# Optimization experiments

Hardware: AMD Instinct MI355X
Metric: run time of the kernel (lower is better)

Reference implementation:

```python
import jax, jax.numpy as jnp
import numpy as np

N_NODES = 50000
N_EDGES = 800000
IN_DIM = 64
HID = 128
OUT_DIM = 64
T_HIST = 8


def setup_inputs() -> dict:
    key = jax.random.key(0)
    ks = jax.random.split(key, 12)
    s = 0.05
    return {
        "node_feats": jax.random.normal(ks[0], (N_NODES, IN_DIM), jnp.float32),
        "history_feats": jax.random.normal(ks[1], (N_NODES, T_HIST, HID), jnp.float32),
        "src": jax.random.randint(ks[2], (N_EDGES,), 0, N_NODES, jnp.int32),
        "dst": jax.random.randint(ks[3], (N_EDGES,), 0, N_NODES, jnp.int32),
        # SAGEConv params (fc_self, fc_neigh share bias as in DGL)
        "W_self": jax.random.normal(ks[4], (IN_DIM, HID), jnp.float32) * s,
        "W_neigh": jax.random.normal(ks[5], (IN_DIM, HID), jnp.float32) * s,
        "b_sage": jnp.zeros((HID,), jnp.float32),
        # LSTM params, PyTorch gate order [i, f, g, o]
        "w_ih": jax.random.normal(ks[6], (HID, 4 * HID), jnp.float32) * s,
        "w_hh": jax.random.normal(ks[7], (HID, 4 * HID), jnp.float32) * s,
        "b_lstm": jnp.zeros((4 * HID,), jnp.float32),
        # classifier
        "W_cls": jax.random.normal(ks[8], (HID, OUT_DIM), jnp.float32) * s,
        "b_cls": jnp.zeros((OUT_DIM,), jnp.float32),
    }


def _lstm_last(x, w_ih, w_hh, b):
    # x: [N, T, H] -> last hidden state [N, H]
    N, T, H = x.shape

    def step(carry, xt):
        h, c = carry
        gates = xt @ w_ih + h @ w_hh + b  # [N, 4H]
        i, f, g, o = jnp.split(gates, 4, axis=-1)
        c = jax.nn.sigmoid(f) * c + jax.nn.sigmoid(i) * jnp.tanh(g)
        h = jax.nn.sigmoid(o) * jnp.tanh(c)
        return (h, c), None

    h0 = jnp.zeros((N, H), x.dtype)
    (h, _), _ = jax.lax.scan(step, (h0, h0), jnp.swapaxes(x, 0, 1))
    return h


def reference(node_feats, history_feats, src, dst, W_self, W_neigh, b_sage,
              w_ih, w_hh, b_lstm, W_cls, b_cls):
    N = node_feats.shape[0]
    # SAGEConv mean aggregation: mean of in-neighbor features per dst node
    msg_sum = jax.ops.segment_sum(node_feats[src], dst, num_segments=N)
    deg = jax.ops.segment_sum(jnp.ones((src.shape[0],), node_feats.dtype),
                              dst, num_segments=N)
    h_neigh = msg_sum / jnp.maximum(deg, 1.0)[:, None]
    h_struct = node_feats @ W_self + h_neigh @ W_neigh + b_sage  # [N, HID]
    # LSTM over history, take last timestep
    h_temp = _lstm_last(history_feats, w_ih, w_hh, b_lstm)  # [N, HID]
    h_combined = h_struct + h_temp
    return h_combined @ W_cls + b_cls  # [N, OUT_DIM]
```

## Files before the change

kernel.cpp:

```cpp
#include <hip/hip_runtime.h>
#include <hip/hip_bf16.h>
#include <stdint.h>

#define N_NODES 50000
#define N_EDGES 800000
#define IN_DIM 64
#define HID 128
#define OUT_DIM 64
#define T_HIST 8

#define NB_SCAN ((N_NODES + 1023) / 1024)

typedef __attribute__((ext_vector_type(8))) short short8;
typedef __attribute__((ext_vector_type(4))) float f32x4;

__device__ __forceinline__ unsigned short f2bf(float x) {
  unsigned int u = __builtin_bit_cast(unsigned int, x);
  unsigned int r = (u + 0x7FFFu + ((u >> 16) & 1u)) >> 16;
  return (unsigned short)r;
}
__device__ __forceinline__ short8 cvt8(float4 a, float4 b) {
  unsigned int w0, w1, w2, w3;
  asm("v_cvt_pk_bf16_f32 %0, %1, %2" : "=v"(w0) : "v"(a.x), "v"(a.y));
  asm("v_cvt_pk_bf16_f32 %0, %1, %2" : "=v"(w1) : "v"(a.z), "v"(a.w));
  asm("v_cvt_pk_bf16_f32 %0, %1, %2" : "=v"(w2) : "v"(b.x), "v"(b.y));
  asm("v_cvt_pk_bf16_f32 %0, %1, %2" : "=v"(w3) : "v"(b.z), "v"(b.w));
  struct { unsigned int a, b, c, d; } s{w0, w1, w2, w3};
  return __builtin_bit_cast(short8, s);
}
__device__ __forceinline__ float sigm(float x) {
  float e = __builtin_amdgcn_exp2f(-1.4426950408889634f * x);
  return __builtin_amdgcn_rcpf(1.f + e);
}
__device__ __forceinline__ float tanh_f(float x) {
  float e = __builtin_amdgcn_exp2f(2.8853900817779268f * x);
  return 1.f - 2.f * __builtin_amdgcn_rcpf(e + 1.f);
}

__global__ void pc_kernel(const float* __restrict__ w_ih, const float* __restrict__ w_hh,
                          const float* __restrict__ W_cls,
                          const float* __restrict__ W_self, const float* __restrict__ W_neigh,
                          const float* __restrict__ b_sage, const float* __restrict__ b_cls,
                          const int* __restrict__ dst,
                          unsigned short* __restrict__ Wt2, unsigned short* __restrict__ Wc2,
                          float* __restrict__ Wsc, float* __restrict__ Wnc,
                          float* __restrict__ bc1, int* __restrict__ cnt) {
  int tid = blockIdx.x * blockDim.x + threadIdx.x;
  int stride = gridDim.x * blockDim.x;
  for (int e = tid; e < N_EDGES; e += stride) atomicAdd(&cnt[dst[e]], 1);
  for (int idx = tid; idx < 256 * 512; idx += stride) {
    int i = idx & 7;
    int lane = (idx >> 3) & 63;
    int F = idx >> 9;
    int q = F >> 5, g = (F >> 3) & 3, kk = F & 7;
    int c = g * 128 + q * 16 + (lane & 15);
    int k = kk * 32 + (lane >> 4) * 8 + i;
    float v = (k < 128) ? w_ih[k * 512 + c] : w_hh[(k - 128) * 512 + c];
    Wt2[idx] = f2bf(v);
  }
  for (int idx = tid; idx < 16 * 512; idx += stride) {
    int i = idx & 7;
    int lane = (idx >> 3) & 63;
    int F = idx >> 9;
    int cb = F >> 2, kk = F & 3;
    int col = cb * 16 + (lane & 15);
    int k = kk * 32 + (lane >> 4) * 8 + i;
    Wc2[idx] = f2bf(W_cls[k * 64 + col]);
  }
  for (int idx = tid; idx < 64 * 64; idx += stride) {
    int k = idx >> 6, c = idx & 63;
    float as = 0.f, an = 0.f;
    for (int m = 0; m < 128; m++) {
      float wc = W_cls[m * 64 + c];
      as += W_self[k * 128 + m] * wc;
      an += W_neigh[k * 128 + m] * wc;
    }
    Wsc[idx] = as;
    Wnc[idx] = an;
  }
  for (int c = tid; c < 64; c += stride) {
    float acc = b_cls[c];
    for (int m = 0; m < 128; m++) acc += b_sage[m] * W_cls[m * 64 + c];
    bc1[c] = acc;
  }
}

__global__ __launch_bounds__(256) void scan1_kernel(const int* __restrict__ cnt,
                                                    int* __restrict__ lexcl, int* __restrict__ btot) {
  __shared__ int sh[256];
  int tid = threadIdx.x;
  int base = blockIdx.x * 1024 + tid * 4;
  int v[4];
  #pragma unroll
  for (int q = 0; q < 4; q++) {
    int i = base + q;
    v[q] = (i < N_NODES) ? cnt[i] : 0;
  }
  int tsum = v[0] + v[1] + v[2] + v[3];
  sh[tid] = tsum;
  __syncthreads();
  int val = tsum;
  for (int off = 1; off < 256; off <<= 1) {
    int x = (tid >= off) ? sh[tid - off] : 0;
    __syncthreads();
    val += x;
    sh[tid] = val;
    __syncthreads();
  }
  int ex = val - tsum;
  if (tid == 255) btot[blockIdx.x] = val;
  #pragma unroll
  for (int q = 0; q < 4; q++) {
    int i = base + q;
    if (i < N_NODES) lexcl[i] = ex;
    ex += v[q];
  }
}

__global__ __launch_bounds__(1024) void scan3_kernel(const int* __restrict__ lexcl,
                                                     const int* __restrict__ btot,
                                                     int* __restrict__ rowstart, int* __restrict__ cursor) {
  int b = blockIdx.x;
  int bs = 0;
  for (int j = 0; j < b; j++) bs += btot[j];
  int i = b * 1024 + threadIdx.x;
  if (i < N_NODES) {
    int rs = lexcl[i] + bs;
    rowstart[i] = rs;
    cursor[i] = rs;
  }
}

__global__ void fill_kernel(const int* __restrict__ src, const int* __restrict__ dst,
                            int* __restrict__ cursor, int* __restrict__ esrc) {
  int e = blockIdx.x * blockDim.x + threadIdx.x;
  if (e < N_EDGES) {
    int d = dst[e];
    int pos = atomicAdd(&cursor[d], 1);
    esrc[pos] = src[e];
  }
}

#define HS_TILE 32
__global__ __launch_bounds__(512) void hstruct_kernel(
    const float* __restrict__ nf, const int* __restrict__ esrc,
    const int* __restrict__ rowstart, const int* __restrict__ cnt,
    const float* __restrict__ Wsc, const float* __restrict__ Wnc, const float* __restrict__ bc1,
    float* __restrict__ out1) {
  __shared__ float s_nf[HS_TILE][IN_DIM + 1];
  __shared__ float s_hn[HS_TILE][IN_DIM + 1];
  int tid = threadIdx.x;
  int node0 = blockIdx.x * HS_TILE;
  for (int i = tid; i < HS_TILE * IN_DIM; i += 512) {
    int r = i >> 6, k = i & 63;
    int node = node0 + r;
    s_nf[r][k] = (node < N_NODES) ? nf[node * 64 + k] : 0.f;
  }
  int wv = tid >> 6, lane = tid & 63;
  for (int r = wv; r < HS_TILE; r += 8) {
    int node = node0 + r;
    float a0 = 0.f, a1 = 0.f, a2 = 0.f, a3 = 0.f;
    int n = 0;
    if (node < N_NODES) {
      n = cnt[node];
      int st = rowstart[node];
      int j = 0;
      for (; j + 4 <= n; j += 4) {
        int s0 = esrc[st + j], s1 = esrc[st + j + 1];
        int s2 = esrc[st + j + 2], s3 = esrc[st + j + 3];
        a0 += nf[s0 * 64 + lane];
        a1 += nf[s1 * 64 + lane];
        a2 += nf[s2 * 64 + lane];
        a3 += nf[s3 * 64 + lane];
      }
      for (; j < n; j++) a0 += nf[esrc[st + j] * 64 + lane];
    }
    s_hn[r][lane] = (a0 + a1 + a2 + a3) * __builtin_amdgcn_rcpf(fmaxf((float)n, 1.f));
  }
  __syncthreads();
  int r = tid & 31;
  int c0 = (tid >> 5) * 4;
  float accs[4] = {0.f, 0.f, 0.f, 0.f};
  for (int k = 0; k < IN_DIM; k++) {
    float a = s_nf[r][k];
    float b = s_hn[r][k];
    float4 w1 = *(const float4*)&Wsc[k * 64 + c0];
    float4 w2 = *(const float4*)&Wnc[k * 64 + c0];
    accs[0] += a * w1.x + b * w2.x;
    accs[1] += a * w1.y + b * w2.y;
    accs[2] += a * w1.z + b * w2.z;
    accs[3] += a * w1.w + b * w2.w;
  }
  int node = node0 + r;
  if (node < N_NODES) {
    #pragma unroll
    for (int i = 0; i < 4; i++)
      out1[(size_t)node * 64 + c0 + i] = accs[i] + bc1[c0 + i];
  }
}

#define LB 64
__global__ __launch_bounds__(512, 2) void lstm_kernel(
    const float* __restrict__ hist,
    const unsigned short* __restrict__ Wt2,
    const unsigned short* __restrict__ Wc2,
    const float* __restrict__ b_lstm,
    const float* __restrict__ out1,
    float* __restrict__ out)
{
  __shared__ alignas(16) unsigned short Abuf[2][64 * 256];

  const int tid = threadIdx.x;
  const int lane = tid & 63;
  const int w = tid >> 6;
  const int l15 = lane & 15;
  const int l4 = lane >> 4;
  const int base = blockIdx.x * LB;
  const int jj = w * 16 + l15;

  short8 Bfr[4][8];
  #pragma unroll
  for (int g = 0; g < 4; g++)
    #pragma unroll
    for (int kk = 0; kk < 8; kk++)
      Bfr[g][kk] = *(const short8*)&Wt2[((w * 32 + g * 8 + kk) * 64 + lane) * 8];

  const float bi  = b_lstm[jj];
  const float bf_ = b_lstm[128 + jj];
  const float bg  = b_lstm[256 + jj];
  const float bo  = b_lstm[384 + jj];

  float c_st[16];
  #pragma unroll
  for (int i = 0; i < 16; i++) c_st[i] = 0.f;

  for (int u = tid; u < 64 * 16; u += 512) {
    int row = u >> 4;
    int kbh = u & 15;
    short8 z = {0,0,0,0,0,0,0,0};
    *(short8*)&Abuf[0][row * 256 + 128 + kbh * 8] = z;
  }
  #pragma unroll
  for (int i2 = 0; i2 < 2; i2++) {
    int u = tid + (i2 << 9);
    int row = u >> 4;
    int kb = u & 15;
    int node = base + row;
    float4 x0 = make_float4(0.f,0.f,0.f,0.f), x1 = make_float4(0.f,0.f,0.f,0.f);
    if (node < N_NODES) {
      const float4* p = (const float4*)&hist[(size_t)node * (T_HIST * HID) + kb * 8];
      x0 = p[0]; x1 = p[1];
    }
    int sb = (kb & 8) | ((kb & 7) ^ (row & 7));
    *(short8*)&Abuf[0][row * 256 + sb * 8] = cvt8(x0, x1);
  }
  __syncthreads();

  float4 xp[4];

  #pragma unroll
  for (int t = 0; t < T_HIST - 1; t++) {
    unsigned short* Acur = &Abuf[t & 1][0];
    unsigned short* Anxt = &Abuf[(t & 1) ^ 1][0];

    #pragma unroll
    for (int i2 = 0; i2 < 2; i2++) {
      int u = tid + (i2 << 9);
      int row = u >> 4;
      int kb = u & 15;
      int node = base + row;
      if (node < N_NODES) {
        const float4* p = (const float4*)&hist[(size_t)node * (T_HIST * HID) + (t + 1) * HID + kb * 8];
        xp[i2 * 2]     = p[0];
        xp[i2 * 2 + 1] = p[1];
      } else {
        xp[i2 * 2]     = make_float4(0.f,0.f,0.f,0.f);
        xp[i2 * 2 + 1] = make_float4(0.f,0.f,0.f,0.f);
      }
    }

    #pragma unroll
    for (int rb = 0; rb < 4; rb++) {
      f32x4 acc[4];
      #pragma unroll
      for (int g = 0; g < 4; g++) { f32x4 z = {0.f,0.f,0.f,0.f}; acc[g] = z; }
      #pragma unroll
      for (int kk = 0; kk < 8; kk++) {
        int row = rb * 16 + l15;
        int kb = kk * 4 + l4;
        int sb = (kb & 24) | ((kb & 7) ^ (row & 7));
        short8 a = *(const short8*)&Acur[row * 256 + sb * 8];
        #pragma unroll
        for (int g = 0; g < 4; g++)
          acc[g] = __builtin_amdgcn_mfma_f32_16x16x32_bf16(a, Bfr[g][kk], acc[g], 0, 0, 0);
      }
      #pragma unroll
      for (int reg = 0; reg < 4; reg++) {
        int r = rb * 4 + reg;
        float gi = sigm(acc[0][reg] + bi);
        float gf = sigm(acc[1][reg] + bf_);
        float gg = tanh_f(acc[2][reg] + bg);
        float go = sigm(acc[3][reg] + bo);
        float c = gf * c_st[r] + gi * gg;
        c_st[r] = c;
        float h = go * tanh_f(c);
        int row = rb * 16 + l4 * 4 + reg;
        int kb = 16 + (jj >> 3);
        int sb = (kb & 24) | ((kb & 7) ^ (row & 7));
        Anxt[row * 256 + sb * 8 + (jj & 7)] = f2bf(h);
      }
      __builtin_amdgcn_sched_barrier(0);
    }

    #pragma unroll
    for (int i2 = 0; i2 < 2; i2++) {
      int u = tid + (i2 << 9);
      int row = u >> 4;
      int kb = u & 15;
      int sb = (kb & 8) | ((kb & 7) ^ (row & 7));
      *(short8*)&Anxt[row * 256 + sb * 8] = cvt8(xp[i2 * 2], xp[i2 * 2 + 1]);
    }
    __syncthreads();
  }

  {
    unsigned short* Acur = &Abuf[1][0];
    unsigned short* Anxt = &Abuf[0][0];

    #pragma unroll
    for (int rb = 0; rb < 4; rb++) {
      f32x4 acc[4];
      #pragma unroll
      for (int g = 0; g < 4; g++) { f32x4 z = {0.f,0.f,0.f,0.f}; acc[g] = z; }
      #pragma unroll
      for (int kk = 0; kk < 8; kk++) {
        int row = rb * 16 + l15;
        int kb = kk * 4 + l4;
        int sb = (kb & 24) | ((kb & 7) ^ (row & 7));
        short8 a = *(const short8*)&Acur[row * 256 + sb * 8];
        #pragma unroll
        for (int g = 0; g < 4; g++)
          acc[g] = __builtin_amdgcn_mfma_f32_16x16x32_bf16(a, Bfr[g][kk], acc[g], 0, 0, 0);
      }
      #pragma unroll
      for (int reg = 0; reg < 4; reg++) {
        int r = rb * 4 + reg;
        float gi = sigm(acc[0][reg] + bi);
        float gf = sigm(acc[1][reg] + bf_);
        float gg = tanh_f(acc[2][reg] + bg);
        float go = sigm(acc[3][reg] + bo);
        float c = gf * c_st[r] + gi * gg;
        float h = go * tanh_f(c);
        int row = rb * 16 + l4 * 4 + reg;
        int kb = jj >> 3;
        int sb = (kb & 8) | ((kb & 7) ^ (row & 7));
        Anxt[row * 256 + sb * 8 + (jj & 7)] = f2bf(h);
      }
      __builtin_amdgcn_sched_barrier(0);
    }
    __syncthreads();

    #pragma unroll
    for (int fi = 0; fi < 2; fi++) {
      int f = w * 2 + fi;
      int rbo = f >> 2, cbo = f & 3;
      int col = cbo * 16 + l15;
      float ov[4];
      #pragma unroll
      for (int reg = 0; reg < 4; reg++) {
        int row = rbo * 16 + l4 * 4 + reg;
        int node = base + row;
        ov[reg] = (node < N_NODES) ? out1[(size_t)node * OUT_DIM + col] : 0.f;
      }
      f32x4 o = {0.f, 0.f, 0.f, 0.f};
      #pragma unroll
      for (int kk = 0; kk < 4; kk++) {
        short8 bv = *(const short8*)&Wc2[((cbo * 4 + kk) * 64 + lane) * 8];
        int row = rbo * 16 + l15;
        int kb = kk * 4 + l4;
        int sb = (kb & 8) | ((kb & 7) ^ (row & 7));
        short8 a = *(const short8*)&Anxt[row * 256 + sb * 8];
        o = __builtin_amdgcn_mfma_f32_16x16x32_bf16(a, bv, o, 0, 0, 0);
      }
      #pragma unroll
      for (int reg = 0; reg < 4; reg++) {
        int row = rbo * 16 + l4 * 4 + reg;
        int node = base + row;
        if (node < N_NODES) out[(size_t)node * OUT_DIM + col] = o[reg] + ov[reg];
      }
    }
  }
}

extern "C" void kernel_launch(void* const* d_in, const int* in_sizes, int n_in,
                              void* d_out, int out_size, void* d_ws, size_t ws_size,
                              hipStream_t stream) {
  (void)in_sizes; (void)n_in; (void)out_size; (void)ws_size;
  const float* node_feats = (const float*)d_in[0];
  const float* hist       = (const float*)d_in[1];
  const int*   src        = (const int*)d_in[2];
  const int*   dst        = (const int*)d_in[3];
  const float* W_self     = (const float*)d_in[4];
  const float* W_neigh    = (const float*)d_in[5];
  const float* b_sage     = (const float*)d_in[6];
  const float* w_ih       = (const float*)d_in[7];
  const float* w_hh       = (const float*)d_in[8];
  const float* b_lstm     = (const float*)d_in[9];
  const float* W_cls      = (const float*)d_in[10];
  const float* b_cls      = (const float*)d_in[11];
  float* out = (float*)d_out;

  char* ws = (char*)d_ws;
  int* cnt        = (int*)(ws);
  int* lexcl      = (int*)(ws + 200192);
  int* rowstart   = (int*)(ws + 400384);
  int* cursor     = (int*)(ws + 600576);
  int* btot       = (int*)(ws + 800768);
  int* esrc       = (int*)(ws + 801792);
  float* out1     = (float*)(ws + 4001792);
  unsigned short* Wt2 = (unsigned short*)(ws + 16801792);
  unsigned short* Wc2 = (unsigned short*)(ws + 17063936);
  float* Wsc      = (float*)(ws + 17080320);
  float* Wnc      = (float*)(ws + 17096704);
  float* bc1      = (float*)(ws + 17113088);

  hipMemsetAsync(cnt, 0, 200000, stream);
  pc_kernel<<<1024, 256, 0, stream>>>(w_ih, w_hh, W_cls, W_self, W_neigh, b_sage, b_cls,
                                      dst, Wt2, Wc2, Wsc, Wnc, bc1, cnt);
  scan1_kernel<<<NB_SCAN, 256, 0, stream>>>(cnt, lexcl, btot);
  scan3_kernel<<<NB_SCAN, 1024, 0, stream>>>(lexcl, btot, rowstart, cursor);
  fill_kernel<<<(N_EDGES + 255) / 256, 256, 0, stream>>>(src, dst, cursor, esrc);
  hstruct_kernel<<<(N_NODES + HS_TILE - 1) / HS_TILE, 512, 0, stream>>>(
      node_feats, esrc, rowstart, cnt, Wsc, Wnc, bc1, out1);
  lstm_kernel<<<(N_NODES + LB - 1) / LB, 512, 0, stream>>>(
      hist, Wt2, Wc2, b_lstm, out1, out);
}
```

Measured before the change: 363.9 us.

## Fuse SAGE neighbor aggregation and projection into LSTM classifier kernel

Removes the separate hstruct kernel and its out1 intermediate. The LSTM kernel now gathers neighbor means and self features per node and writes them as bf16 into unused columns of the shared A tile. An extra set of MFMAs then applies the pre-combined (W_self|W_neigh)@W_cls matrix, which is stored in bf16 fragment layout. This saves one launch and the write and re-read of a 50000x64 float buffer, but the irregular gather is now serialized inside the LSTM blocks and node and neighbor features are rounded to bf16.

New measurement: 376.5 us. 1.03x slower.

```diff
diff --git a/kernel.cpp b/kernel.cpp
--- a/kernel.cpp
+++ b/kernel.cpp
@@ -43,7 +43,7 @@
                           const float* __restrict__ b_sage, const float* __restrict__ b_cls,
                           const int* __restrict__ dst,
                           unsigned short* __restrict__ Wt2, unsigned short* __restrict__ Wc2,
-                          float* __restrict__ Wsc, float* __restrict__ Wnc,
+                          unsigned short* __restrict__ Wsnc2,
                           float* __restrict__ bc1, int* __restrict__ cnt) {
   int tid = blockIdx.x * blockDim.x + threadIdx.x;
   int stride = gridDim.x * blockDim.x;
@@ -67,16 +67,17 @@
     int k = kk * 32 + (lane >> 4) * 8 + i;
     Wc2[idx] = f2bf(W_cls[k * 64 + col]);
   }
-  for (int idx = tid; idx < 64 * 64; idx += stride) {
-    int k = idx >> 6, c = idx & 63;
-    float as = 0.f, an = 0.f;
-    for (int m = 0; m < 128; m++) {
-      float wc = W_cls[m * 64 + c];
-      as += W_self[k * 128 + m] * wc;
-      an += W_neigh[k * 128 + m] * wc;
-    }
-    Wsc[idx] = as;
-    Wnc[idx] = an;
+  for (int idx = tid; idx < 16 * 512; idx += stride) {
+    int i = idx & 7;
+    int lane = (idx >> 3) & 63;
+    int F = idx >> 9;
+    int cb = F >> 2, kk = F & 3;
+    int col = cb * 16 + (lane & 15);
+    int k = kk * 32 + (lane >> 4) * 8 + i;
+    const float* Wrow = (k < 64) ? &W_self[k * 128] : &W_neigh[(k - 64) * 128];
+    float v = 0.f;
+    for (int m = 0; m < 128; m++) v += Wrow[m] * W_cls[m * 64 + col];
+    Wsnc2[idx] = f2bf(v);
   }
   for (int c = tid; c < 64; c += stride) {
     float acc = b_cls[c];
@@ -141,71 +142,18 @@
   }
 }
 
-#define HS_TILE 32
-__global__ __launch_bounds__(512) void hstruct_kernel(
-    const float* __restrict__ nf, const int* __restrict__ esrc,
-    const int* __restrict__ rowstart, const int* __restrict__ cnt,
-    const float* __restrict__ Wsc, const float* __restrict__ Wnc, const float* __restrict__ bc1,
-    float* __restrict__ out1) {
-  __shared__ float s_nf[HS_TILE][IN_DIM + 1];
-  __shared__ float s_hn[HS_TILE][IN_DIM + 1];
-  int tid = threadIdx.x;
-  int node0 = blockIdx.x * HS_TILE;
-  for (int i = tid; i < HS_TILE * IN_DIM; i += 512) {
-    int r = i >> 6, k = i & 63;
-    int node = node0 + r;
-    s_nf[r][k] = (node < N_NODES) ? nf[node * 64 + k] : 0.f;
-  }
-  int wv = tid >> 6, lane = tid & 63;
-  for (int r = wv; r < HS_TILE; r += 8) {
-    int node = node0 + r;
-    float a0 = 0.f, a1 = 0.f, a2 = 0.f, a3 = 0.f;
-    int n = 0;
-    if (node < N_NODES) {
-      n = cnt[node];
-      int st = rowstart[node];
-      int j = 0;
-      for (; j + 4 <= n; j += 4) {
-        int s0 = esrc[st + j], s1 = esrc[st + j + 1];
-        int s2 = esrc[st + j + 2], s3 = esrc[st + j + 3];
-        a0 += nf[s0 * 64 + lane];
-        a1 += nf[s1 * 64 + lane];
-        a2 += nf[s2 * 64 + lane];
-        a3 += nf[s3 * 64 + lane];
-      }
-      for (; j < n; j++) a0 += nf[esrc[st + j] * 64 + lane];
-    }
-    s_hn[r][lane] = (a0 + a1 + a2 + a3) * __builtin_amdgcn_rcpf(fmaxf((float)n, 1.f));
-  }
-  __syncthreads();
-  int r = tid & 31;
-  int c0 = (tid >> 5) * 4;
-  float accs[4] = {0.f, 0.f, 0.f, 0.f};
-  for (int k = 0; k < IN_DIM; k++) {
-    float a = s_nf[r][k];
-    float b = s_hn[r][k];
-    float4 w1 = *(const float4*)&Wsc[k * 64 + c0];
-    float4 w2 = *(const float4*)&Wnc[k * 64 + c0];
-    accs[0] += a * w1.x + b * w2.x;
-    accs[1] += a * w1.y + b * w2.y;
-    accs[2] += a * w1.z + b * w2.z;
-    accs[3] += a * w1.w + b * w2.w;
-  }
-  int node = node0 + r;
-  if (node < N_NODES) {
-    #pragma unroll
-    for (int i = 0; i < 4; i++)
-      out1[(size_t)node * 64 + c0 + i] = accs[i] + bc1[c0 + i];
-  }
-}
-
 #define LB 64
 __global__ __launch_bounds__(512, 2) void lstm_kernel(
     const float* __restrict__ hist,
     const unsigned short* __restrict__ Wt2,
     const unsigned short* __restrict__ Wc2,
+    const unsigned short* __restrict__ Wsnc2,
     const float* __restrict__ b_lstm,
-    const float* __restrict__ out1,
+    const float* __restrict__ nf,
+    const int* __restrict__ esrc,
+    const int* __restrict__ rowstart,
+    const int* __restrict__ cnt,
+    const float* __restrict__ bc1,
     float* __restrict__ out)
 {
   __shared__ alignas(16) unsigned short Abuf[2][64 * 256];
@@ -358,6 +306,43 @@
       }
       __builtin_amdgcn_sched_barrier(0);
     }
+
+    float nfreg[8], hnreg[8];
+    #pragma unroll
+    for (int rr = 0; rr < 8; rr++) {
+      int node = base + w * 8 + rr;
+      nfreg[rr] = (node < N_NODES) ? nf[node * 64 + lane] : 0.f;
+    }
+    for (int rr = 0; rr < 8; rr++) {
+      int node = base + w * 8 + rr;
+      float a0 = 0.f, a1 = 0.f, a2 = 0.f, a3 = 0.f;
+      int n = 0;
+      if (node < N_NODES) {
+        n = cnt[node];
+        int st = rowstart[node];
+        int j = 0;
+        for (; j + 4 <= n; j += 4) {
+          int s0 = esrc[st + j], s1 = esrc[st + j + 1];
+          int s2 = esrc[st + j + 2], s3 = esrc[st + j + 3];
+          a0 += nf[s0 * 64 + lane];
+          a1 += nf[s1 * 64 + lane];
+          a2 += nf[s2 * 64 + lane];
+          a3 += nf[s3 * 64 + lane];
+        }
+        for (; j < n; j++) a0 += nf[esrc[st + j] * 64 + lane];
+      }
+      hnreg[rr] = (a0 + a1 + a2 + a3) * __builtin_amdgcn_rcpf(fmaxf((float)n, 1.f));
+    }
+    #pragma unroll
+    for (int rr = 0; rr < 8; rr++) {
+      int row = w * 8 + rr;
+      int kbn = 16 + (lane >> 3);
+      int sbn = (kbn & 24) | ((kbn & 7) ^ (row & 7));
+      Anxt[row * 256 + sbn * 8 + (lane & 7)] = f2bf(nfreg[rr]);
+      int kbh = 24 + (lane >> 3);
+      int sbh = (kbh & 24) | ((kbh & 7) ^ (row & 7));
+      Anxt[row * 256 + sbh * 8 + (lane & 7)] = f2bf(hnreg[rr]);
+    }
     __syncthreads();
 
     #pragma unroll
@@ -365,13 +350,6 @@
       int f = w * 2 + fi;
       int rbo = f >> 2, cbo = f & 3;
       int col = cbo * 16 + l15;
-      float ov[4];
-      #pragma unroll
-      for (int reg = 0; reg < 4; reg++) {
-        int row = rbo * 16 + l4 * 4 + reg;
-        int node = base + row;
-        ov[reg] = (node < N_NODES) ? out1[(size_t)node * OUT_DIM + col] : 0.f;
-      }
       f32x4 o = {0.f, 0.f, 0.f, 0.f};
       #pragma unroll
       for (int kk = 0; kk < 4; kk++) {
@@ -383,10 +361,20 @@
         o = __builtin_amdgcn_mfma_f32_16x16x32_bf16(a, bv, o, 0, 0, 0);
       }
       #pragma unroll
+      for (int kk = 0; kk < 4; kk++) {
+        short8 bv = *(const short8*)&Wsnc2[((cbo * 4 + kk) * 64 + lane) * 8];
+        int row = rbo * 16 + l15;
+        int kb = 16 + kk * 4 + l4;
+        int sb = (kb & 24) | ((kb & 7) ^ (row & 7));
+        short8 a = *(const short8*)&Anxt[row * 256 + sb * 8];
+        o = __builtin_amdgcn_mfma_f32_16x16x32_bf16(a, bv, o, 0, 0, 0);
+      }
+      float bcl = bc1[col];
+      #pragma unroll
       for (int reg = 0; reg < 4; reg++) {
         int row = rbo * 16 + l4 * 4 + reg;
         int node = base + row;
-        if (node < N_NODES) out[(size_t)node * OUT_DIM + col] = o[reg] + ov[reg];
+        if (node < N_NODES) out[(size_t)node * OUT_DIM + col] = o[reg] + bcl;
       }
     }
   }
@@ -417,21 +405,17 @@
   int* cursor     = (int*)(ws + 600576);
   int* btot       = (int*)(ws + 800768);
   int* esrc       = (int*)(ws + 801792);
-  float* out1     = (float*)(ws + 4001792);
-  unsigned short* Wt2 = (unsigned short*)(ws + 16801792);
-  unsigned short* Wc2 = (unsigned short*)(ws + 17063936);
-  float* Wsc      = (float*)(ws + 17080320);
-  float* Wnc      = (float*)(ws + 17096704);
-  float* bc1      = (float*)(ws + 17113088);
+  unsigned short* Wt2   = (unsigned short*)(ws + 4001792);
+  unsigned short* Wc2   = (unsigned short*)(ws + 4263936);
+  unsigned short* Wsnc2 = (unsigned short*)(ws + 4280320);
+  float* bc1      = (float*)(ws + 4296704);
 
   hipMemsetAsync(cnt, 0, 200000, stream);
   pc_kernel<<<1024, 256, 0, stream>>>(w_ih, w_hh, W_cls, W_self, W_neigh, b_sage, b_cls,
-                                      dst, Wt2, Wc2, Wsc, Wnc, bc1, cnt);
+                                      dst, Wt2, Wc2, Wsnc2, bc1, cnt);
   scan1_kernel<<<NB_SCAN, 256, 0, stream>>>(cnt, lexcl, btot);
   scan3_kernel<<<NB_SCAN, 1024, 0, stream>>>(lexcl, btot, rowstart, cursor);
   fill_kernel<<<(N_EDGES + 255) / 256, 256, 0, stream>>>(src, dst, cursor, esrc);
-  hstruct_kernel<<<(N_NODES + HS_TILE - 1) / HS_TILE, 512, 0, stream>>>(
-      node_feats, esrc, rowstart, cnt, Wsc, Wnc, bc1, out1);
   lstm_kernel<<<(N_NODES + LB - 1) / LB, 512, 0, stream>>>(
-      hist, Wt2, Wc2, b_lstm, out1, out);
-}
+      hist, Wt2, Wc2, Wsnc2, b_lstm, node_feats, esrc, rowstart, cnt, bc1, out);
+}
```

## Split LSTM gates across wave pairs with LDS gate exchange, 1024-thread blocks

Applied to the files above, without the earlier changes.

The LSTM kernel now runs 16 waves per block, each wave pair sharing a 16-column slice, with each wave computing two of the four gate groups. The half of the gate results a wave does not own is exchanged through a new shared-memory buffer, so each wave applies the nonlinearities for half of the rows. This halves the per-wave B-fragment registers and cell state, aiming for higher occupancy and more parallelism. The cost is an extra barrier per timestep, extra LDS traffic and usage, and the time loop is no longer unrolled.

New measurement: 444.5 us. +22.1%, slower.

```diff
diff --git a/kernel.cpp b/kernel.cpp
--- a/kernel.cpp
+++ b/kernel.cpp
@@ -200,7 +200,7 @@
 }
 
 #define LB 64
-__global__ __launch_bounds__(512, 2) void lstm_kernel(
+__global__ __launch_bounds__(1024, 4) void lstm_kernel(
     const float* __restrict__ hist,
     const unsigned short* __restrict__ Wt2,
     const unsigned short* __restrict__ Wc2,
@@ -209,42 +209,36 @@
     float* __restrict__ out)
 {
   __shared__ alignas(16) unsigned short Abuf[2][64 * 256];
+  __shared__ float Gbuf[2][2][32][132];
 
   const int tid = threadIdx.x;
   const int lane = tid & 63;
   const int w = tid >> 6;
+  const int q = w >> 1;
+  const int h = w & 1;
   const int l15 = lane & 15;
   const int l4 = lane >> 4;
   const int base = blockIdx.x * LB;
-  const int jj = w * 16 + l15;
-
-  short8 Bfr[4][8];
+  const int jj = q * 16 + l15;
+
+  short8 Bfr[2][8];
   #pragma unroll
-  for (int g = 0; g < 4; g++)
+  for (int gg = 0; gg < 2; gg++)
     #pragma unroll
     for (int kk = 0; kk < 8; kk++)
-      Bfr[g][kk] = *(const short8*)&Wt2[((w * 32 + g * 8 + kk) * 64 + lane) * 8];
-
-  const float bi  = b_lstm[jj];
-  const float bf_ = b_lstm[128 + jj];
-  const float bg  = b_lstm[256 + jj];
-  const float bo  = b_lstm[384 + jj];
-
-  float c_st[16];
+      Bfr[gg][kk] = *(const short8*)&Wt2[((q * 32 + (2 * h + gg) * 8 + kk) * 64 + lane) * 8];
+
+  const float bA = b_lstm[(2 * h + 0) * 128 + jj];
+  const float bB = b_lstm[(2 * h + 1) * 128 + jj];
+
+  float c_st[8];
   #pragma unroll
-  for (int i = 0; i < 16; i++) c_st[i] = 0.f;
-
-  for (int u = tid; u < 64 * 16; u += 512) {
-    int row = u >> 4;
-    int kbh = u & 15;
+  for (int i = 0; i < 8; i++) c_st[i] = 0.f;
+
+  {
+    int row = tid >> 4, kb = tid & 15;
     short8 z = {0,0,0,0,0,0,0,0};
-    *(short8*)&Abuf[0][row * 256 + 128 + kbh * 8] = z;
-  }
-  #pragma unroll
-  for (int i2 = 0; i2 < 2; i2++) {
-    int u = tid + (i2 << 9);
-    int row = u >> 4;
-    int kb = u & 15;
+    *(short8*)&Abuf[0][row * 256 + 128 + kb * 8] = z;
     int node = base + row;
     float4 x0 = make_float4(0.f,0.f,0.f,0.f), x1 = make_float4(0.f,0.f,0.f,0.f);
     if (node < N_NODES) {
@@ -256,138 +250,110 @@
   }
   __syncthreads();
 
-  float4 xp[4];
-
-  #pragma unroll
-  for (int t = 0; t < T_HIST - 1; t++) {
+  #pragma unroll 1
+  for (int t = 0; t < T_HIST; t++) {
     unsigned short* Acur = &Abuf[t & 1][0];
     unsigned short* Anxt = &Abuf[(t & 1) ^ 1][0];
 
-    #pragma unroll
-    for (int i2 = 0; i2 < 2; i2++) {
-      int u = tid + (i2 << 9);
-      int row = u >> 4;
-      int kb = u & 15;
-      int node = base + row;
-      if (node < N_NODES) {
-        const float4* p = (const float4*)&hist[(size_t)node * (T_HIST * HID) + (t + 1) * HID + kb * 8];
-        xp[i2 * 2]     = p[0];
-        xp[i2 * 2 + 1] = p[1];
-      } else {
-        xp[i2 * 2]     = make_float4(0.f,0.f,0.f,0.f);
-        xp[i2 * 2 + 1] = make_float4(0.f,0.f,0.f,0.f);
-      }
-    }
+    f32x4 ownA[2][2];
 
     #pragma unroll
     for (int rb = 0; rb < 4; rb++) {
-      f32x4 acc[4];
-      #pragma unroll
-      for (int g = 0; g < 4; g++) { f32x4 z = {0.f,0.f,0.f,0.f}; acc[g] = z; }
+      f32x4 a0 = {0.f,0.f,0.f,0.f}, a1 = {0.f,0.f,0.f,0.f};
       #pragma unroll
       for (int kk = 0; kk < 8; kk++) {
         int row = rb * 16 + l15;
         int kb = kk * 4 + l4;
         int sb = (kb & 24) | ((kb & 7) ^ (row & 7));
         short8 a = *(const short8*)&Acur[row * 256 + sb * 8];
+        a0 = __builtin_amdgcn_mfma_f32_16x16x32_bf16(a, Bfr[0][kk], a0, 0, 0, 0);
+        a1 = __builtin_amdgcn_mfma_f32_16x16x32_bf16(a, Bfr[1][kk], a1, 0, 0, 0);
+      }
+      bool own = (h == 0) ? (rb < 2) : (rb >= 2);
+      if (own) {
+        ownA[rb & 1][0] = a0;
+        ownA[rb & 1][1] = a1;
+      } else {
+        int r32b = (h == 0) ? (rb - 2) * 16 : rb * 16;
         #pragma unroll
-        for (int g = 0; g < 4; g++)
-          acc[g] = __builtin_amdgcn_mfma_f32_16x16x32_bf16(a, Bfr[g][kk], acc[g], 0, 0, 0);
+        for (int reg = 0; reg < 4; reg++) {
+          int r32 = r32b + l4 * 4 + reg;
+          Gbuf[h][0][r32][jj] = a0[reg] + bA;
+          Gbuf[h][1][r32][jj] = a1[reg] + bB;
+        }
       }
+      __builtin_amdgcn_sched_barrier(0);
+    }
+    __syncthreads();
+
+    #pragma unroll
+    for (int p = 0; p < 2; p++) {
       #pragma unroll
       for (int reg = 0; reg < 4; reg++) {
-        int r = rb * 4 + reg;
-        float gi = sigm(acc[0][reg] + bi);
-        float gf = sigm(acc[1][reg] + bf_);
-        float gg = tanh_f(acc[2][reg] + bg);
-        float go = sigm(acc[3][reg] + bo);
-        float c = gf * c_st[r] + gi * gg;
-        c_st[r] = c;
-        float h = go * tanh_f(c);
-        int row = rb * 16 + l4 * 4 + reg;
-        int kb = 16 + (jj >> 3);
-        int sb = (kb & 24) | ((kb & 7) ^ (row & 7));
-        Anxt[row * 256 + sb * 8 + (jj & 7)] = f2bf(h);
+        int r32 = p * 16 + l4 * 4 + reg;
+        int row = h * 32 + r32;
+        int ci = p * 4 + reg;
+        float o0 = ownA[p][0][reg] + bA;
+        float o1 = ownA[p][1][reg] + bB;
+        float g0 = Gbuf[1 - h][0][r32][jj];
+        float g1 = Gbuf[1 - h][1][r32][jj];
+        float gi, gf, gg_, go;
+        if (h == 0) { gi = sigm(o0); gf = sigm(o1); gg_ = tanh_f(g0); go = sigm(g1); }
+        else        { gi = sigm(g0); gf = sigm(g1); gg_ = tanh_f(o0); go = sigm(o1); }
+        float c = gf * c_st[ci] + gi * gg_;
+        c_st[ci] = c;
+        float hv = go * tanh_f(c);
+        if (t < T_HIST - 1) {
+          int kb = 16 + (jj >> 3);
+          int sb = (kb & 24) | ((kb & 7) ^ (row & 7));
+          Anxt[row * 256 + sb * 8 + (jj & 7)] = f2bf(hv);
+        } else {
+          int kb = jj >> 3;
+          int sb = (kb & 8) | ((kb & 7) ^ (row & 7));
+          Anxt[row * 256 + sb * 8 + (jj & 7)] = f2bf(hv);
+        }
       }
-      __builtin_amdgcn_sched_barrier(0);
-    }
-
-    #pragma unroll
-    for (int i2 = 0; i2 < 2; i2++) {
-      int u = tid + (i2 << 9);
-      int row = u >> 4;
-      int kb = u & 15;
+    }
+    if (t < T_HIST - 1) {
+      int row = tid >> 4, kb = tid & 15;
+      int node = base + row;
+      float4 x0 = make_float4(0.f,0.f,0.f,0.f), x1 = make_float4(0.f,0.f,0.f,0.f);
+      if (node < N_NODES) {
+        const float4* p = (const float4*)&hist[(size_t)node * (T_HIST * HID) + (t + 1) * HID + kb * 8];
+        x0 = p[0]; x1 = p[1];
+      }
       int sb = (kb & 8) | ((kb & 7) ^ (row & 7));
-      *(short8*)&Anxt[row * 256 + sb * 8] = cvt8(xp[i2 * 2], xp[i2 * 2 + 1]);
+      *(short8*)&Anxt[row * 256 + sb * 8] = cvt8(x0, x1);
     }
     __syncthreads();
   }
 
   {
-    unsigned short* Acur = &Abuf[1][0];
-    unsigned short* Anxt = &Abuf[0][0];
-
-    #pragma unroll
-    for (int rb = 0; rb < 4; rb++) {
-      f32x4 acc[4];
-      #pragma unroll
-      for (int g = 0; g < 4; g++) { f32x4 z = {0.f,0.f,0.f,0.f}; acc[g] = z; }
-      #pragma unroll
-      for (int kk = 0; kk < 8; kk++) {
-        int row = rb * 16 + l15;
-        int kb = kk * 4 + l4;
-        int sb = (kb & 24) | ((kb & 7) ^ (row & 7));
-        short8 a = *(const short8*)&Acur[row * 256 + sb * 8];
-        #pragma unroll
-        for (int g = 0; g < 4; g++)
-          acc[g] = __builtin_amdgcn_mfma_f32_16x16x32_bf16(a, Bfr[g][kk], acc[g], 0, 0, 0);
-      }
-      #pragma unroll
-      for (int reg = 0; reg < 4; reg++) {
-        int r = rb * 4 + reg;
-        float gi = sigm(acc[0][reg] + bi);
-        float gf = sigm(acc[1][reg] + bf_);
-        float gg = tanh_f(acc[2][reg] + bg);
-        float go = sigm(acc[3][reg] + bo);
-        float c = gf * c_st[r] + gi * gg;
-        float h = go * tanh_f(c);
-        int row = rb * 16 + l4 * 4 + reg;
-        int kb = jj >> 3;
-        int sb = (kb & 8) | ((kb & 7) ^ (row & 7));
-        Anxt[row * 256 + sb * 8 + (jj & 7)] = f2bf(h);
-      }
-      __builtin_amdgcn_sched_barrier(0);
-    }
-    __syncthreads();
-
-    #pragma unroll
-    for (int fi = 0; fi < 2; fi++) {
-      int f = w * 2 + fi;
-      int rbo = f >> 2, cbo = f & 3;
-      int col = cbo * 16 + l15;
-      float ov[4];
-      #pragma unroll
-      for (int reg = 0; reg < 4; reg++) {
-        int row = rbo * 16 + l4 * 4 + reg;
-        int node = base + row;
-        ov[reg] = (node < N_NODES) ? out1[(size_t)node * OUT_DIM + col] : 0.f;
-      }
-      f32x4 o = {0.f, 0.f, 0.f, 0.f};
-      #pragma unroll
-      for (int kk = 0; kk < 4; kk++) {
-        short8 bv = *(const short8*)&Wc2[((cbo * 4 + kk) * 64 + lane) * 8];
-        int row = rbo * 16 + l15;
-        int kb = kk * 4 + l4;
-        int sb = (kb & 8) | ((kb & 7) ^ (row & 7));
-        short8 a = *(const short8*)&Anxt[row * 256 + sb * 8];
-        o = __builtin_amdgcn_mfma_f32_16x16x32_bf16(a, bv, o, 0, 0, 0);
-      }
-      #pragma unroll
-      for (int reg = 0; reg < 4; reg++) {
-        int row = rbo * 16 + l4 * 4 + reg;
-        int node = base + row;
-        if (node < N_NODES) out[(size_t)node * OUT_DIM + col] = o[reg] + ov[reg];
-      }
+    const unsigned short* Afin = &Abuf[0][0];
+    int rbo = w >> 2, cbo = w & 3;
+    int col = cbo * 16 + l15;
+    float ov[4];
+    #pragma unroll
+    for (int reg = 0; reg < 4; reg++) {
+      int row = rbo * 16 + l4 * 4 + reg;
+      int node = base + row;
+      ov[reg] = (node < N_NODES) ? out1[(size_t)node * OUT_DIM + col] : 0.f;
+    }
+    f32x4 o = {0.f, 0.f, 0.f, 0.f};
+    #pragma unroll
+    for (int kk = 0; kk < 4; kk++) {
+      short8 bv = *(const short8*)&Wc2[((cbo * 4 + kk) * 64 + lane) * 8];
+      int row = rbo * 16 + l15;
+      int kb = kk * 4 + l4;
+      int sb = (kb & 8) | ((kb & 7) ^ (row & 7));
+      short8 a = *(const short8*)&Afin[row * 256 + sb * 8];
+      o = __builtin_amdgcn_mfma_f32_16x16x32_bf16(a, bv, o, 0, 0, 0);
+    }
+    #pragma unroll
+    for (int reg = 0; reg < 4; reg++) {
+      int row = rbo * 16 + l4 * 4 + reg;
+      int node = base + row;
+      if (node < N_NODES) out[(size_t)node * OUT_DIM + col] = o[reg] + ov[reg];
     }
   }
 }
@@ -432,6 +398,6 @@
   fill_kernel<<<(N_EDGES + 255) / 256, 256, 0, stream>>>(src, dst, cursor, esrc);
   hstruct_kernel<<<(N_NODES + HS_TILE - 1) / HS_TILE, 512, 0, stream>>>(
       node_feats, esrc, rowstart, cnt, Wsc, Wnc, bc1, out1);
-  lstm_kernel<<<(N_NODES + LB - 1) / LB, 512, 0, stream>>>(
+  lstm_kernel<<<(N_NODES + LB - 1) / LB, 1024, 0, stream>>>(
       hist, Wt2, Wc2, b_lstm, out1, out);
 }
```
